# Performance work log

Measured on AMD Instinct MI355X. Metric: run time of the kernel, lower is better.

## Reference

```python
import jax, jax.numpy as jnp
import numpy as np

# Mamba hyperparams (standard defaults: expand=2, d_conv=4, dt_rank=ceil(d_model/16))
D_MODEL = 256
D_STATE = 16
D_CONV = 4
D_INNER = 2 * D_MODEL  # 512
DT_RANK = (D_MODEL + 15) // 16  # 16
B, H, W = 2, 64, 64


def setup_inputs() -> dict:
    key = jax.random.key(0)
    ks = jax.random.split(key, 8)
    def rnd(k, shape, scale):
        return jax.random.normal(k, shape, jnp.float32) * scale
    A_log = jnp.log(jnp.tile(jnp.arange(1, D_STATE + 1, dtype=jnp.float32), (D_INNER, 1)))
    return {
        "x": jax.random.normal(ks[0], (B, D_MODEL, H, W), jnp.float32),
        "W_in": rnd(ks[1], (D_MODEL, 2 * D_INNER), 0.02),
        "conv_w": rnd(ks[2], (D_INNER, 1, D_CONV), 0.1),
        "conv_b": jnp.zeros((D_INNER,), jnp.float32),
        "W_x": rnd(ks[3], (D_INNER, DT_RANK + 2 * D_STATE), 0.02),
        "W_dt": rnd(ks[4], (DT_RANK, D_INNER), 0.02),
        "b_dt": rnd(ks[5], (D_INNER,), 0.1),
        "A_log": A_log,
        "D": jnp.ones((D_INNER,), jnp.float32),
        "W_out": rnd(ks[6], (D_INNER, D_MODEL), 0.02),
    }


def _mamba(z, W_in, conv_w, conv_b, W_x, W_dt, b_dt, A_log, Dp, W_out):
    # z: (Bt, L, d_model)
    Bt = z.shape[0]
    xz = z @ W_in                              # (Bt, L, 2*d_inner)
    xm, gate = jnp.split(xz, 2, axis=-1)
    # causal depthwise conv1d (kernel D_CONV, left-padded)
    xc = jnp.transpose(xm, (0, 2, 1))          # (Bt, d_inner, L)
    xc = jnp.pad(xc, ((0, 0), (0, 0), (D_CONV - 1, 0)))
    xc = jax.lax.conv_general_dilated(
        xc, conv_w, (1,), 'VALID',
        dimension_numbers=('NCH', 'OIH', 'NCH'),
        feature_group_count=D_INNER)
    xc = xc + conv_b[None, :, None]
    xs = jax.nn.silu(jnp.transpose(xc, (0, 2, 1)))   # (Bt, L, d_inner)
    dbl = xs @ W_x                                     # (Bt, L, dt_rank + 2*d_state)
    dt = jax.nn.softplus(dbl[..., :DT_RANK] @ W_dt + b_dt)  # (Bt, L, d_inner)
    Bm = dbl[..., DT_RANK:DT_RANK + D_STATE]           # (Bt, L, d_state)
    Cm = dbl[..., DT_RANK + D_STATE:]                  # (Bt, L, d_state)
    A = -jnp.exp(A_log)                                # (d_inner, d_state)

    def step(state, ins):
        dt_t, B_t, C_t, x_t = ins                      # (Bt,d_inner),(Bt,d_state),(Bt,d_state),(Bt,d_inner)
        dA = jnp.exp(dt_t[..., None] * A)              # (Bt, d_inner, d_state)
        state = dA * state + (dt_t * x_t)[..., None] * B_t[:, None, :]
        y_t = jnp.einsum('bds,bs->bd', state, C_t)
        return state, y_t

    tm = lambda a: jnp.moveaxis(a, 1, 0)               # time-major
    init = jnp.zeros((Bt, D_INNER, D_STATE), z.dtype)
    _, ys = jax.lax.scan(step, init, (tm(dt), tm(Bm), tm(Cm), tm(xs)))
    y = jnp.moveaxis(ys, 0, 1) + xs * Dp               # skip via D
    y = y * jax.nn.silu(gate)
    return y @ W_out                                   # (Bt, L, d_model)


def reference(x, W_in, conv_w, conv_b, W_x, W_dt, b_dt, A_log, D, W_out):
    b, c, h, w = x.shape
    l = h * w
    # four scan directions: identity, flip w, flip h, flip both
    zs = jnp.stack([x,
                    jnp.flip(x, 3),
                    jnp.flip(x, 2),
                    jnp.flip(x, (2, 3))], axis=0)       # (4, b, c, h, w)
    zs = zs.reshape(4 * b, c, l).transpose(0, 2, 1)     # (4b, l, c)
    y = _mamba(zs, W_in, conv_w, conv_b, W_x, W_dt, b_dt, A_log, D, W_out)
    y = y.transpose(0, 2, 1).reshape(4, b, c, h, w)
    y0 = y[0]
    y1 = jnp.flip(y[1], 3)
    y2 = jnp.flip(y[2], 2)
    y3 = jnp.flip(y[3], (2, 3))
    return (y0 + y1 + y2 + y3) / 4.0
```

## Files before the change

### kernel.cpp

```cpp
#include <hip/hip_runtime.h>
#include <cstdint>
#include <cstddef>

#define LSEQ 4096
#define DI   512
#define NSTATE 16
#define TC 32
#define NCH 128

#define XM_OFF    0
#define GATE_OFF  16777216
#define XS_OFF    33554432
#define DBL_OFF   50331648
#define SPLIT_OFF 51904512
#define AP_OFF    0
#define PS_OFF    8388608

typedef unsigned short u16;
typedef __attribute__((ext_vector_type(8))) short s8v;
typedef __attribute__((ext_vector_type(4))) float f4v;
typedef __attribute__((ext_vector_type(4))) unsigned int u32x4;

#ifndef __has_builtin
#define __has_builtin(x) 0
#endif
#if __has_builtin(__builtin_amdgcn_global_load_lds)
#define USE_GLL 1
#else
#define USE_GLL 0
#endif

__device__ __forceinline__ float silu_f(float v) {
  return v * __frcp_rn(1.f + __expf(-v));
}
__device__ __forceinline__ float softplus_f(float v) {
  return fmaxf(v, 0.f) + __logf(1.f + __expf(-fabsf(v)));
}
__device__ __forceinline__ u16 bf16_hi(float v) {
  unsigned u = __float_as_uint(v);
  return (u16)((u + 0x7fffu + ((u >> 16) & 1u)) >> 16);
}
__device__ __forceinline__ float bf16_f(u16 h) { return __uint_as_float(((unsigned)h) << 16); }

__device__ __forceinline__ void gld16(const u16* g, u16* l, int lane) {
#if USE_GLL
  __builtin_amdgcn_global_load_lds((const __attribute__((address_space(1))) void*)g,
                                   (__attribute__((address_space(3))) void*)l, 16, 0, 0);
#else
  *(u32x4*)(l + lane * 8) = *(const u32x4*)g;
#endif
}

__device__ __forceinline__ void pow_ladder(float r, float* a) {
  const float r2 = r * r, r4 = r2 * r2, r8 = r4 * r4;
  a[0] = r;        a[1] = r2;       a[2] = r2 * r;   a[3] = r4;
  a[4] = r4 * r;   a[5] = r4 * r2;  a[6] = r4 * a[2]; a[7] = r8;
  a[8] = r8 * r;   a[9] = r8 * r2;  a[10] = r8 * a[2]; a[11] = r8 * r4;
  a[12] = r8 * a[4]; a[13] = r8 * a[5]; a[14] = r8 * a[6]; a[15] = r8 * r8;
}

__global__ __launch_bounds__(256) void k_split(const float* __restrict__ in,
                                               u16* __restrict__ oh,
                                               u16* __restrict__ ol,
                                               int R, int C) {
  __shared__ float tile[64][65];
  const size_t zoff = (size_t)blockIdx.z * R * C;
  in += zoff; oh += zoff; ol += zoff;
  const int c0 = blockIdx.x << 6, r0 = blockIdx.y << 6;
  const int tid = threadIdx.x;
  const int tx = tid & 63, ty = tid >> 6;
#pragma unroll
  for (int i = 0; i < 16; ++i) {
    const int r = ty + (i << 2);
    tile[r][tx] = in[(size_t)(r0 + r) * C + c0 + tx];
  }
  __syncthreads();
#pragma unroll
  for (int i = 0; i < 16; ++i) {
    const int cc = ty + (i << 2);
    const float v = tile[tx][cc];
    const u16 h = bf16_hi(v);
    const size_t o = (size_t)(c0 + cc) * R + r0 + tx;
    oh[o] = h;
    ol[o] = bf16_hi(v - bf16_f(h));
  }
}

__global__ __launch_bounds__(256) void k_gemm_in_mfma(const u16* __restrict__ xTh,
                                                      const u16* __restrict__ xTl,
                                                      const u16* __restrict__ Wh,
                                                      const u16* __restrict__ Wl,
                                                      float* __restrict__ xm,
                                                      float* __restrict__ gate) {
  __shared__ __attribute__((aligned(16))) u16 lds[4 * 128 * 32];
  u16* Ah = lds;
  u16* Al = lds + 4096;
  u16* Bh = lds + 8192;
  u16* Bl = lds + 12288;
  const int rt = blockIdx.x;
  const int nt = blockIdx.y;
  const int seq = rt >> 5, hl2 = rt & 31;
  const int b = seq & 1, dir = seq >> 1;
  const int tid = threadIdx.x;
  const int lane = tid & 63, wid = tid >> 6;
  const int wr = wid >> 1, wc = wid & 1;

  const u16* gsrc = (wid == 0) ? xTh : (wid == 1) ? xTl : (wid == 2) ? Wh : Wl;
  u16* ldst = lds + (wid << 12);
  size_t roff[8];
#pragma unroll
  for (int i = 0; i < 8; ++i) {
    const int r = (i << 4) + (lane >> 2);
    size_t off;
    if (wid < 2) {
      const int hl = (hl2 << 1) + (r >> 6), w = r & 63;
      const int hp = (dir & 2) ? 63 - hl : hl;
      const int wp = (dir & 1) ? 63 - w : w;
      off = ((size_t)((b << 12) + (hp << 6) + wp)) << 8;
    } else {
      off = ((size_t)((nt << 7) + r)) << 8;
    }
    roff[i] = off + ((lane & 3) << 3);
  }

  f4v acc[4][4];
  const f4v z4 = {0.f, 0.f, 0.f, 0.f};
#pragma unroll
  for (int m = 0; m < 4; ++m)
#pragma unroll
    for (int n = 0; n < 4; ++n) acc[m][n] = z4;

  const int fr = lane & 15;
  const int kg = (lane >> 4) << 3;

  for (int kc = 0; kc < 256; kc += 32) {
    __syncthreads();
#pragma unroll
    for (int i = 0; i < 8; ++i) gld16(gsrc + roff[i] + kc, ldst + (i << 9), lane);
    __syncthreads();
    s8v Afh[4], Afl[4], Bfh[4], Bfl[4];
#pragma unroll
    for (int m = 0; m < 4; ++m) {
      const int row = (wr << 6) + (m << 4) + fr;
      Afh[m] = *(const s8v*)&Ah[row * 32 + kg];
      Afl[m] = *(const s8v*)&Al[row * 32 + kg];
    }
#pragma unroll
    for (int n = 0; n < 4; ++n) {
      const int row = (wc << 6) + (n << 4) + fr;
      Bfh[n] = *(const s8v*)&Bh[row * 32 + kg];
      Bfl[n] = *(const s8v*)&Bl[row * 32 + kg];
    }
#pragma unroll
    for (int m = 0; m < 4; ++m)
#pragma unroll
      for (int n = 0; n < 4; ++n) {
        acc[m][n] = __builtin_amdgcn_mfma_f32_16x16x32_bf16(Afh[m], Bfh[n], acc[m][n], 0, 0, 0);
        acc[m][n] = __builtin_amdgcn_mfma_f32_16x16x32_bf16(Afh[m], Bfl[n], acc[m][n], 0, 0, 0);
        acc[m][n] = __builtin_amdgcn_mfma_f32_16x16x32_bf16(Afl[m], Bfh[n], acc[m][n], 0, 0, 0);
      }
  }
  const int rg = (lane >> 4) << 2;
  float* obuf = (nt & 4) ? gate : xm;
  const int ncol = (nt & 3) << 7;
  float* obase = obuf + ((size_t)((rt << 7) + (wr << 6) + rg)) * DI + ncol + (wc << 6) + fr;
#pragma unroll
  for (int m = 0; m < 4; ++m)
#pragma unroll
    for (int n = 0; n < 4; ++n)
#pragma unroll
      for (int j = 0; j < 4; ++j)
        obase[(size_t)((m << 4) + j) * DI + (n << 4)] = acc[m][n][j];
}

__global__ __launch_bounds__(256) void k_conv(const float* __restrict__ xmb,
                                              const float* __restrict__ cw,
                                              const float* __restrict__ cb,
                                              float* __restrict__ xs) {
  const int t0  = blockIdx.x << 4;
  const int seq = blockIdx.y;
  const int d   = (blockIdx.z << 8) + threadIdx.x;
  const float* xm = xmb + (size_t)seq * LSEQ * DI + d;
  const float w0 = cw[d * 4], w1 = cw[d * 4 + 1], w2 = cw[d * 4 + 2], w3 = cw[d * 4 + 3];
  const float bias = cb[d];
  float r0 = (t0 >= 3) ? xm[(size_t)(t0 - 3) * DI] : 0.f;
  float r1 = (t0 >= 2) ? xm[(size_t)(t0 - 2) * DI] : 0.f;
  float r2 = (t0 >= 1) ? xm[(size_t)(t0 - 1) * DI] : 0.f;
  float* orow = xs + ((size_t)seq * LSEQ + t0) * DI + d;
#pragma unroll
  for (int i = 0; i < 16; ++i) {
    const float r3 = xm[(size_t)(t0 + i) * DI];
    const float v = fmaf(w0, r0, fmaf(w1, r1, fmaf(w2, r2, fmaf(w3, r3, bias))));
    orow[(size_t)i * DI] = silu_f(v);
    r0 = r1; r1 = r2; r2 = r3;
  }
}

__global__ __launch_bounds__(256) void k_gemm_x(const float* __restrict__ xs,
                                                const float* __restrict__ Wx,
                                                float* __restrict__ dbl) {
  __shared__ float xsh[16][512];
  const int rb  = blockIdx.x;
  const int tid = threadIdx.x;
  const int r = tid >> 4, k4 = tid & 15;
  const float* src = xs + (size_t)rb * 16 * DI;
#pragma unroll
  for (int i = 0; i < 8; ++i) {
    const int k = (i << 6) + (k4 << 2);
    *(float4*)&xsh[r][k] = *(const float4*)&src[(size_t)r * DI + k];
  }
  __syncthreads();
  if (tid < 192) {
    const int col = tid % 48;
    const int rg  = tid / 48;
    float a0 = 0.f, a1 = 0.f, a2 = 0.f, a3 = 0.f;
    for (int k = 0; k < 512; k += 4) {
      float wv0 = Wx[(size_t)(k + 0) * 48 + col];
      float wv1 = Wx[(size_t)(k + 1) * 48 + col];
      float wv2 = Wx[(size_t)(k + 2) * 48 + col];
      float wv3 = Wx[(size_t)(k + 3) * 48 + col];
      const float4 x0 = *(const float4*)&xsh[rg * 4 + 0][k];
      const float4 x1 = *(const float4*)&xsh[rg * 4 + 1][k];
      const float4 x2 = *(const float4*)&xsh[rg * 4 + 2][k];
      const float4 x3 = *(const float4*)&xsh[rg * 4 + 3][k];
      a0 = fmaf(x0.x, wv0, fmaf(x0.y, wv1, fmaf(x0.z, wv2, fmaf(x0.w, wv3, a0))));
      a1 = fmaf(x1.x, wv0, fmaf(x1.y, wv1, fmaf(x1.z, wv2, fmaf(x1.w, wv3, a1))));
      a2 = fmaf(x2.x, wv0, fmaf(x2.y, wv1, fmaf(x2.z, wv2, fmaf(x2.w, wv3, a2))));
      a3 = fmaf(x3.x, wv0, fmaf(x3.y, wv1, fmaf(x3.z, wv2, fmaf(x3.w, wv3, a3))));
    }
    const size_t base = ((size_t)rb * 16 + rg * 4) * 48 + col;
    dbl[base] = a0; dbl[base + 48] = a1; dbl[base + 96] = a2; dbl[base + 144] = a3;
  }
}

__global__ __launch_bounds__(256) void k_scan1(const float* __restrict__ xs,
                                               const float* __restrict__ dbl,
                                               const float* __restrict__ Wdt,
                                               const float* __restrict__ bdt,
                                               const float* __restrict__ Alog,
                                               float* __restrict__ aprod,
                                               float* __restrict__ pstate) {
  __shared__ float dsh[TC * 48];
  const int ch = blockIdx.x, seq = blockIdx.y;
  const int tid = threadIdx.x;
  const int d = (blockIdx.z << 8) + tid;
  const int t0 = ch * TC;
  const float* dsrc = dbl + ((size_t)seq * LSEQ + t0) * 48;
#pragma unroll
  for (int i = 0; i < 6; ++i) dsh[tid + (i << 8)] = dsrc[tid + (i << 8)];
  float wdt[16], Aa[16], st[16], P[16];
#pragma unroll
  for (int k = 0; k < 16; ++k) wdt[k] = Wdt[(size_t)k * DI + d];
  const float bd = bdt[d];
  bool fast = true;
#pragma unroll
  for (int s = 0; s < NSTATE; ++s) {
    const float Av = __expf(Alog[d * NSTATE + s]);
    Aa[s] = -Av;
    fast = fast && (fabsf(Av - (float)(s + 1)) < 1e-3f);
    st[s] = 0.f; P[s] = 1.f;
  }
  const float* xsrc = xs + ((size_t)seq * LSEQ + t0) * DI + d;
  __syncthreads();
  if (fast) {
    float Rp = 1.f;
    for (int t = 0; t < TC; ++t) {
      const float* dr = &dsh[t * 48];
      float dtp = bd;
#pragma unroll
      for (int k = 0; k < 16; ++k) dtp = fmaf(dr[k], wdt[k], dtp);
      const float dtv = softplus_f(dtp);
      const float u = dtv * xsrc[(size_t)t * DI];
      const float r = __expf(-dtv);
      float a[16];
      pow_ladder(r, a);
      Rp *= r;
#pragma unroll
      for (int s = 0; s < NSTATE; ++s) st[s] = fmaf(a[s], st[s], u * dr[16 + s]);
    }
    pow_ladder(Rp, P);
  } else {
    for (int t = 0; t < TC; ++t) {
      const float* dr = &dsh[t * 48];
      float dtp = bd;
#pragma unroll
      for (int k = 0; k < 16; ++k) dtp = fmaf(dr[k], wdt[k], dtp);
      const float dtv = softplus_f(dtp);
      const float u = dtv * xsrc[(size_t)t * DI];
#pragma unroll
      for (int s = 0; s < NSTATE; ++s) {
        const float a = __expf(dtv * Aa[s]);
        st[s] = fmaf(a, st[s], u * dr[16 + s]);
        P[s] *= a;
      }
    }
  }
  float* ap = aprod  + (((size_t)seq * NCH + ch) * DI + d) * NSTATE;
  float* pp = pstate + (((size_t)seq * NCH + ch) * DI + d) * NSTATE;
#pragma unroll
  for (int s = 0; s < NSTATE; s += 4) {
    *(float4*)&ap[s] = make_float4(P[s], P[s + 1], P[s + 2], P[s + 3]);
    *(float4*)&pp[s] = make_float4(st[s], st[s + 1], st[s + 2], st[s + 3]);
  }
}

__global__ __launch_bounds__(256) void k_scan2(const float* __restrict__ aprod,
                                               float* __restrict__ pstate) {
  const int flat = blockIdx.x * 256 + threadIdx.x;
  const int seq = flat >> 13;
  const int rem = flat & 8191;
  const size_t stride = (size_t)DI * NSTATE;
  const size_t base = (size_t)seq * NCH * stride + rem;
  float h = 0.f;
  for (int ch = 0; ch < NCH; ++ch) {
    const size_t o = base + (size_t)ch * stride;
    const float a = aprod[o];
    const float bsum = pstate[o];
    pstate[o] = h;
    h = fmaf(a, h, bsum);
  }
}

__global__ __launch_bounds__(256) void k_scan3(const float* __restrict__ gate,
                                               float* __restrict__ xs,
                                               const float* __restrict__ dbl,
                                               const float* __restrict__ Wdt,
                                               const float* __restrict__ bdt,
                                               const float* __restrict__ Alog,
                                               const float* __restrict__ Dv,
                                               const float* __restrict__ hinit) {
  __shared__ float dsh[TC * 48];
  const int ch = blockIdx.x, seq = blockIdx.y;
  const int tid = threadIdx.x;
  const int d = (blockIdx.z << 8) + tid;
  const int t0 = ch * TC;
  const float* dsrc = dbl + ((size_t)seq * LSEQ + t0) * 48;
#pragma unroll
  for (int i = 0; i < 6; ++i) dsh[tid + (i << 8)] = dsrc[tid + (i << 8)];
  float wdt[16], Aa[16], st[16];
#pragma unroll
  for (int k = 0; k < 16; ++k) wdt[k] = Wdt[(size_t)k * DI + d];
  const float bd = bdt[d];
  const float Dp = Dv[d];
  const float* hp = hinit + (((size_t)seq * NCH + ch) * DI + d) * NSTATE;
  bool fast = true;
#pragma unroll
  for (int s = 0; s < NSTATE; ++s) {
    const float Av = __expf(Alog[d * NSTATE + s]);
    Aa[s] = -Av;
    fast = fast && (fabsf(Av - (float)(s + 1)) < 1e-3f);
    st[s] = hp[s];
  }
  float* xrow = xs + ((size_t)seq * LSEQ + t0) * DI + d;
  const float* grow = gate + ((size_t)seq * LSEQ + t0) * DI + d;
  __syncthreads();
  if (fast) {
    for (int t = 0; t < TC; ++t) {
      const float* dr = &dsh[t * 48];
      float dtp = bd;
#pragma unroll
      for (int k = 0; k < 16; ++k) dtp = fmaf(dr[k], wdt[k], dtp);
      const float dtv = softplus_f(dtp);
      const float xsv = xrow[(size_t)t * DI];
      const float u = dtv * xsv;
      const float r = __expf(-dtv);
      float a[16];
      pow_ladder(r, a);
      float y = 0.f;
#pragma unroll
      for (int s = 0; s < NSTATE; ++s) {
        st[s] = fmaf(a[s], st[s], u * dr[16 + s]);
        y = fmaf(st[s], dr[32 + s], y);
      }
      y = fmaf(xsv, Dp, y);
      y *= silu_f(grow[(size_t)t * DI]);
      xrow[(size_t)t * DI] = y;
    }
  } else {
    for (int t = 0; t < TC; ++t) {
      const float* dr = &dsh[t * 48];
      float dtp = bd;
#pragma unroll
      for (int k = 0; k < 16; ++k) dtp = fmaf(dr[k], wdt[k], dtp);
      const float dtv = softplus_f(dtp);
      const float xsv = xrow[(size_t)t * DI];
      const float u = dtv * xsv;
      float y = 0.f;
#pragma unroll
      for (int s = 0; s < NSTATE; ++s) {
        const float a = __expf(dtv * Aa[s]);
        st[s] = fmaf(a, st[s], u * dr[16 + s]);
        y = fmaf(st[s], dr[32 + s], y);
      }
      y = fmaf(xsv, Dp, y);
      y *= silu_f(grow[(size_t)t * DI]);
      xrow[(size_t)t * DI] = y;
    }
  }
}

__global__ __launch_bounds__(256, 2) void k_gemm_out(const float* __restrict__ y,
                                                     const float* __restrict__ Wout,
                                                     float* __restrict__ out) {
  __shared__ float Ash[64 * 33];
  __shared__ float Bsh[64 * 132];
  const int bx = blockIdx.x;
  const int b = bx >> 7, tt = bx & 127;
  const int t0 = tt << 5;
  const int c0 = blockIdx.y << 7;
  const int tid = threadIdx.x;
  const int h = t0 >> 6, hf = 63 - h;
  const int w0 = t0 & 63;
  const int ar = tid >> 3, ak = tid & 7;
  const int w = w0 + ar, wf = 63 - w;
  const size_t row0 = ((size_t)(0 + b) * LSEQ + (h << 6) + w) * DI;
  const size_t row1 = ((size_t)(2 + b) * LSEQ + (h << 6) + wf) * DI;
  const size_t row2 = ((size_t)(4 + b) * LSEQ + (hf << 6) + w) * DI;
  const size_t row3 = ((size_t)(6 + b) * LSEQ + (hf << 6) + wf) * DI;
  const int bk = tid >> 3, bc = tid & 7;
  const int tx = tid & 31, cy = tid >> 5;
  float acc[16];
#pragma unroll
  for (int j = 0; j < 16; ++j) acc[j] = 0.f;

  for (int kc = 0; kc < 512; kc += 64) {
#pragma unroll
    for (int f = 0; f < 2; ++f) {
      const int kl = (ak << 3) + (f << 2);
      const int k = kl + kc;
      const float4 v0 = *(const float4*)&y[row0 + k];
      const float4 v1 = *(const float4*)&y[row1 + k];
      const float4 v2 = *(const float4*)&y[row2 + k];
      const float4 v3 = *(const float4*)&y[row3 + k];
      Ash[(kl + 0) * 33 + ar] = 0.25f * (v0.x + v1.x + v2.x + v3.x);
      Ash[(kl + 1) * 33 + ar] = 0.25f * (v0.y + v1.y + v2.y + v3.y);
      Ash[(kl + 2) * 33 + ar] = 0.25f * (v0.z + v1.z + v2.z + v3.z);
      Ash[(kl + 3) * 33 + ar] = 0.25f * (v0.w + v1.w + v2.w + v3.w);
    }
#pragma unroll
    for (int rr = 0; rr < 2; ++rr) {
      const int kk = bk + (rr << 5);
#pragma unroll
      for (int i = 0; i < 4; ++i) {
        const int c = (bc << 2) + (i << 5);
        *(float4*)&Bsh[kk * 132 + c] =
            *(const float4*)&Wout[(size_t)(kc + kk) * 256 + c0 + c];
      }
    }
    __syncthreads();
#pragma unroll
    for (int kk = 0; kk < 64; ++kk) {
      const float a = Ash[kk * 33 + tx];
      const float* bp = &Bsh[kk * 132 + (cy << 4)];
      const float4 b0 = *(const float4*)&bp[0];
      const float4 b1 = *(const float4*)&bp[4];
      const float4 b2 = *(const float4*)&bp[8];
      const float4 b3 = *(const float4*)&bp[12];
      acc[0]  = fmaf(a, b0.x, acc[0]);   acc[1]  = fmaf(a, b0.y, acc[1]);
      acc[2]  = fmaf(a, b0.z, acc[2]);   acc[3]  = fmaf(a, b0.w, acc[3]);
      acc[4]  = fmaf(a, b1.x, acc[4]);   acc[5]  = fmaf(a, b1.y, acc[5]);
      acc[6]  = fmaf(a, b1.z, acc[6]);   acc[7]  = fmaf(a, b1.w, acc[7]);
      acc[8]  = fmaf(a, b2.x, acc[8]);   acc[9]  = fmaf(a, b2.y, acc[9]);
      acc[10] = fmaf(a, b2.z, acc[10]);  acc[11] = fmaf(a, b2.w, acc[11]);
      acc[12] = fmaf(a, b3.x, acc[12]);  acc[13] = fmaf(a, b3.y, acc[13]);
      acc[14] = fmaf(a, b3.z, acc[14]);  acc[15] = fmaf(a, b3.w, acc[15]);
    }
    __syncthreads();
  }
#pragma unroll
  for (int j = 0; j < 16; ++j) {
    const int c = c0 + (cy << 4) + j;
    out[((size_t)b * 256 + c) * LSEQ + t0 + tx] = acc[j];
  }
}

extern "C" void kernel_launch(void* const* d_in, const int* in_sizes, int n_in,
                              void* d_out, int out_size, void* d_ws, size_t ws_size,
                              hipStream_t stream) {
  const float* x     = (const float*)d_in[0];
  const float* W_in  = (const float*)d_in[1];
  const float* convw = (const float*)d_in[2];
  const float* convb = (const float*)d_in[3];
  const float* W_x   = (const float*)d_in[4];
  const float* W_dt  = (const float*)d_in[5];
  const float* b_dt  = (const float*)d_in[6];
  const float* A_log = (const float*)d_in[7];
  const float* Dvec  = (const float*)d_in[8];
  const float* W_out = (const float*)d_in[9];
  float* out = (float*)d_out;

  float* ws   = (float*)d_ws;
  float* xm   = ws + XM_OFF;
  float* gate = ws + GATE_OFF;
  float* xs   = ws + XS_OFF;
  float* dbl  = ws + DBL_OFF;
  float* ap   = ws + AP_OFF;
  float* ps   = ws + PS_OFF;

  u16* xTh   = (u16*)(ws + SPLIT_OFF);
  u16* xTl   = xTh + 2097152;
  u16* WinTh = xTl + 2097152;
  u16* WinTl = WinTh + 262144;

  k_split<<<dim3(64, 4, 2), 256, 0, stream>>>(x, xTh, xTl, 256, 4096);
  k_split<<<dim3(16, 4, 1), 256, 0, stream>>>(W_in, WinTh, WinTl, 256, 1024);
  k_gemm_in_mfma<<<dim3(256, 8), 256, 0, stream>>>(xTh, xTl, WinTh, WinTl, xm, gate);
  k_conv<<<dim3(256, 8, 2), 256, 0, stream>>>(xm, convw, convb, xs);
  k_gemm_x<<<dim3(2048), 256, 0, stream>>>(xs, W_x, dbl);
  k_scan1<<<dim3(NCH, 8, 2), 256, 0, stream>>>(xs, dbl, W_dt, b_dt, A_log, ap, ps);
  k_scan2<<<dim3(256), 256, 0, stream>>>(ap, ps);
  k_scan3<<<dim3(NCH, 8, 2), 256, 0, stream>>>(gate, xs, dbl, W_dt, b_dt, A_log, Dvec, ps);
  k_gemm_out<<<dim3(256, 2), 256, 0, stream>>>(xs, W_out, out);
}
```

Measured before the change: 412.5 us.

## Fuse causal conv into x-projection GEMM and simplify softplus/decay math

Merges the depthwise causal conv+SiLU kernel into the W_x projection kernel. Each block now computes its 16 conv rows straight into shared memory (still writing xs to global for later scans), so xs is no longer re-read from global and one launch is dropped. Separately, in both scan kernels the decay r=exp(-softplus(dtp)) is computed directly as 1/(1+exp(dtp)), with dt recovered as -log(r). This replaces a softplus and an exp with an rcp, an exp and a log. The new formula clamps at 80, which may slightly change precision for large dtp.

```diff
diff --git a/kernel.cpp b/kernel.cpp
--- a/kernel.cpp
+++ b/kernel.cpp
@@ -173,41 +173,38 @@
         obase[(size_t)((m << 4) + j) * DI + (n << 4)] = acc[m][n][j];
 }
 
-__global__ __launch_bounds__(256) void k_conv(const float* __restrict__ xmb,
-                                              const float* __restrict__ cw,
-                                              const float* __restrict__ cb,
-                                              float* __restrict__ xs) {
-  const int t0  = blockIdx.x << 4;
-  const int seq = blockIdx.y;
-  const int d   = (blockIdx.z << 8) + threadIdx.x;
-  const float* xm = xmb + (size_t)seq * LSEQ * DI + d;
-  const float w0 = cw[d * 4], w1 = cw[d * 4 + 1], w2 = cw[d * 4 + 2], w3 = cw[d * 4 + 3];
-  const float bias = cb[d];
-  float r0 = (t0 >= 3) ? xm[(size_t)(t0 - 3) * DI] : 0.f;
-  float r1 = (t0 >= 2) ? xm[(size_t)(t0 - 2) * DI] : 0.f;
-  float r2 = (t0 >= 1) ? xm[(size_t)(t0 - 1) * DI] : 0.f;
-  float* orow = xs + ((size_t)seq * LSEQ + t0) * DI + d;
-#pragma unroll
-  for (int i = 0; i < 16; ++i) {
-    const float r3 = xm[(size_t)(t0 + i) * DI];
-    const float v = fmaf(w0, r0, fmaf(w1, r1, fmaf(w2, r2, fmaf(w3, r3, bias))));
-    orow[(size_t)i * DI] = silu_f(v);
-    r0 = r1; r1 = r2; r2 = r3;
-  }
-}
-
-__global__ __launch_bounds__(256) void k_gemm_x(const float* __restrict__ xs,
-                                                const float* __restrict__ Wx,
-                                                float* __restrict__ dbl) {
+__global__ __launch_bounds__(256) void k_convx(const float* __restrict__ xmb,
+                                               const float* __restrict__ cw,
+                                               const float* __restrict__ cb,
+                                               const float* __restrict__ Wx,
+                                               float* __restrict__ xs,
+                                               float* __restrict__ dbl) {
   __shared__ float xsh[16][512];
   const int rb  = blockIdx.x;
   const int tid = threadIdx.x;
-  const int r = tid >> 4, k4 = tid & 15;
-  const float* src = xs + (size_t)rb * 16 * DI;
-#pragma unroll
-  for (int i = 0; i < 8; ++i) {
-    const int k = (i << 6) + (k4 << 2);
-    *(float4*)&xsh[r][k] = *(const float4*)&src[(size_t)r * DI + k];
+  const int r0g = rb << 4;
+  const int t0  = r0g & 4095;
+#pragma unroll
+  for (int half = 0; half < 2; ++half) {
+    const int d = tid + (half << 8);
+    const float w0 = cw[d * 4], w1 = cw[d * 4 + 1], w2 = cw[d * 4 + 2], w3 = cw[d * 4 + 3];
+    const float bias = cb[d];
+    float r0 = 0.f, r1 = 0.f, r2 = 0.f;
+    if (t0 != 0) {
+      r0 = xmb[((size_t)r0g - 3) * DI + d];
+      r1 = xmb[((size_t)r0g - 2) * DI + d];
+      r2 = xmb[((size_t)r0g - 1) * DI + d];
+    }
+    float* xsg = xs + (size_t)r0g * DI + d;
+#pragma unroll
+    for (int i = 0; i < 16; ++i) {
+      const float r3 = xmb[(size_t)(r0g + i) * DI + d];
+      const float v = fmaf(w0, r0, fmaf(w1, r1, fmaf(w2, r2, fmaf(w3, r3, bias))));
+      const float sv = silu_f(v);
+      xsh[i][d] = sv;
+      xsg[(size_t)i * DI] = sv;
+      r0 = r1; r1 = r2; r2 = r3;
+    }
   }
   __syncthreads();
   if (tid < 192) {
@@ -269,9 +266,9 @@
       float dtp = bd;
 #pragma unroll
       for (int k = 0; k < 16; ++k) dtp = fmaf(dr[k], wdt[k], dtp);
-      const float dtv = softplus_f(dtp);
+      const float r = __frcp_rn(1.f + __expf(fminf(dtp, 80.f)));
+      const float dtv = -__logf(r);
       const float u = dtv * xsrc[(size_t)t * DI];
-      const float r = __expf(-dtv);
       float a[16];
       pow_ladder(r, a);
       Rp *= r;
@@ -360,10 +357,10 @@
       float dtp = bd;
 #pragma unroll
       for (int k = 0; k < 16; ++k) dtp = fmaf(dr[k], wdt[k], dtp);
-      const float dtv = softplus_f(dtp);
+      const float r = __frcp_rn(1.f + __expf(fminf(dtp, 80.f)));
+      const float dtv = -__logf(r);
       const float xsv = xrow[(size_t)t * DI];
       const float u = dtv * xsv;
-      const float r = __expf(-dtv);
       float a[16];
       pow_ladder(r, a);
       float y = 0.f;
@@ -505,8 +502,7 @@
   k_split<<<dim3(64, 4, 2), 256, 0, stream>>>(x, xTh, xTl, 256, 4096);
   k_split<<<dim3(16, 4, 1), 256, 0, stream>>>(W_in, WinTh, WinTl, 256, 1024);
   k_gemm_in_mfma<<<dim3(256, 8), 256, 0, stream>>>(xTh, xTl, WinTh, WinTl, xm, gate);
-  k_conv<<<dim3(256, 8, 2), 256, 0, stream>>>(xm, convw, convb, xs);
-  k_gemm_x<<<dim3(2048), 256, 0, stream>>>(xs, W_x, dbl);
+  k_convx<<<dim3(2048), 256, 0, stream>>>(xm, convw, convb, W_x, xs, dbl);
   k_scan1<<<dim3(NCH, 8, 2), 256, 0, stream>>>(xs, dbl, W_dt, b_dt, A_log, ap, ps);
   k_scan2<<<dim3(256), 256, 0, stream>>>(ap, ps);
   k_scan3<<<dim3(NCH, 8, 2), 256, 0, stream>>>(gate, xs, dbl, W_dt, b_dt, A_log, Dvec, ps);
```

Result: no change. 406.3 us (-1.5%).
